# Optimization experiments

Measured on AMD Instinct MI355X. Metric: run time of the kernel, lower is better.

## Reference

```python
import math
import jax, jax.numpy as jnp
import numpy as np

B, L, HID = 2, 2048, 2048
H = 16
D = HID // H  # 128
EPS = 1e-6
ROPE_BASE = 10000.0
BETA_MIN, BETA_MAX = 0.8, 0.9995


def _rope_cache(seq_len, dim):
    half = dim // 2
    inv_freq = 1.0 / (ROPE_BASE ** (jnp.arange(half, dtype=jnp.float32) / float(half)))
    t = jnp.arange(seq_len, dtype=jnp.float32)
    freqs = t[:, None] * inv_freq[None, :]  # [L, half]
    return jnp.cos(freqs), jnp.sin(freqs)


def _apply_rope(x, cos, sin):
    # x: [B, H, L, D]; cos/sin: [L, D//2]
    half = x.shape[-1] // 2
    xe, xo = x[..., :half], x[..., half:]
    c = cos[None, None]
    s = sin[None, None]
    return jnp.concatenate([xe * c - xo * s, xe * s + xo * c], axis=-1)


def setup_inputs() -> dict:
    key = jax.random.key(0)
    ks = jax.random.split(key, 6)
    sc = 1.0 / math.sqrt(HID)  # ~ xavier scale
    return {
        "x": jax.random.normal(ks[0], (B, L, HID), jnp.float32),
        "Wq": jax.random.normal(ks[1], (HID, HID), jnp.float32) * sc,
        "Wk": jax.random.normal(ks[2], (HID, HID), jnp.float32) * sc,
        "Wv": jax.random.normal(ks[3], (HID, HID), jnp.float32) * sc,
        "Wg": jax.random.normal(ks[4], (HID, H), jnp.float32) * sc,
        "bg": jnp.full((H,), math.log(0.98 / (1.0 - 0.98)), jnp.float32),
        "Wo": jax.random.normal(ks[5], (HID, HID), jnp.float32) * sc,
        "bo": jnp.zeros((HID,), jnp.float32),
    }


def _deltanet(x, Wq, Wk, Wv, Wg, bg, Wo, bo):
    Bb, Ll, _ = x.shape
    split = lambda t: t.reshape(Bb, Ll, H, D).transpose(0, 2, 1, 3)  # [B,H,L,D]
    q = split(x @ Wq)
    k = split(x @ Wk)
    v = split(x @ Wv)

    cos, sin = _rope_cache(Ll, D)
    q = _apply_rope(q, cos, sin)
    k = _apply_rope(k, cos, sin)

    beta = jax.nn.sigmoid(x @ Wg + bg)                # [B,L,H]
    beta = jnp.clip(beta, BETA_MIN, BETA_MAX).transpose(0, 2, 1)  # [B,H,L]

    phi_q = jax.nn.elu(q) + 1.0
    phi_k = jax.nn.elu(k) + 1.0

    # time-major for scan
    pq = phi_q.transpose(2, 0, 1, 3)  # [L,B,H,D]
    pk = phi_k.transpose(2, 0, 1, 3)
    vt = v.transpose(2, 0, 1, 3)
    bt = beta.transpose(2, 0, 1)      # [L,B,H]

    S0 = jnp.zeros((Bb, H, D, D), jnp.float32)
    z0 = jnp.zeros((Bb, H, D), jnp.float32)

    def step(carry, inp):
        S, z = carry
        pq_t, pk_t, v_t, b_t = inp
        S = S * b_t[..., None, None] + pk_t[..., :, None] * v_t[..., None, :]
        z = z * b_t[..., None] + pk_t
        numer = jnp.einsum('bhd,bhde->bhe', pq_t, S)
        denom = jnp.sum(pq_t * z, axis=-1, keepdims=True) + EPS
        return (S, z), numer / denom

    (_, _), y = jax.lax.scan(step, (S0, z0), (pq, pk, vt, bt))  # y: [L,B,H,D]
    y = y.transpose(1, 0, 2, 3).reshape(Bb, Ll, HID)  # [B,L,H*D]
    return y @ Wo + bo


def reference(x, Wq, Wk, Wv, Wg, bg, Wo, bo):
    return _deltanet(x, Wq, Wk, Wv, Wg, bg, Wo, bo)
```

## Files before the change

### kernel.cpp

```cpp
#include <hip/hip_runtime.h>


typedef __attribute__((ext_vector_type(8))) short short8;
typedef __attribute__((ext_vector_type(4))) float f32x4;

__device__ __forceinline__ unsigned short f2bf(float f) {
  unsigned u = __float_as_uint(f);
  u += 0x7fffu + ((u >> 16) & 1u);
  return (unsigned short)(u >> 16);
}
__device__ __forceinline__ float bf2f(unsigned short s) {
  return __uint_as_float(((unsigned)s) << 16);
}
__device__ __forceinline__ float phi_elu1(float x) {
  return x > 0.f ? x + 1.f : expf(x);
}
__device__ __forceinline__ void gl_lds16(const void* g, void* l) {
  __builtin_amdgcn_global_load_lds(
      (const __attribute__((address_space(1))) void*)g,
      (__attribute__((address_space(3))) void*)l, 16, 0, 0);
}

__global__ __launch_bounds__(256)
void k_cast(const float* __restrict__ x, unsigned short* __restrict__ xb) {
  int i = (blockIdx.x * 256 + threadIdx.x) * 4;
  float4 f = *(const float4*)(x + i);
  uint2 p;
  p.x = (unsigned)f2bf(f.x) | ((unsigned)f2bf(f.y) << 16);
  p.y = (unsigned)f2bf(f.z) | ((unsigned)f2bf(f.w) << 16);
  *(uint2*)(xb + i) = p;
}

__global__ __launch_bounds__(256)
void k_transw(const float* __restrict__ Wq, const float* __restrict__ Wk,
              const float* __restrict__ Wv, const float* __restrict__ Wo,
              const float* __restrict__ Wg,
              unsigned short* __restrict__ Wt, unsigned short* __restrict__ Wot,
              unsigned short* __restrict__ Wgt16) {
  const int z = blockIdx.z;
  if (z == 4) {
    if (blockIdx.y != 0) return;
    int idx = blockIdx.x * 256 + threadIdx.x;
    int h = idx >> 9, k4 = (idx & 511) * 4;
    uint2 p;
    p.x = (unsigned)f2bf(Wg[(k4 + 0) * 16 + h]) | ((unsigned)f2bf(Wg[(k4 + 1) * 16 + h]) << 16);
    p.y = (unsigned)f2bf(Wg[(k4 + 2) * 16 + h]) | ((unsigned)f2bf(Wg[(k4 + 3) * 16 + h]) << 16);
    *(uint2*)(Wgt16 + (size_t)h * 2048 + k4) = p;
    return;
  }
  const float* W = (z == 0) ? Wq : (z == 1) ? Wk : (z == 2) ? Wv : Wo;
  unsigned short* out = (z < 3) ? (Wt + (size_t)z * 2048 * 2048) : Wot;
  __shared__ float tile[64][65];
  const int n0 = blockIdx.x * 64;
  const int k0 = blockIdx.y * 64;
  const int tx = threadIdx.x & 63;
  const int ty = threadIdx.x >> 6;
#pragma unroll
  for (int rl = 0; rl < 16; ++rl) {
    int kk = rl * 4 + ty;
    tile[kk][tx] = W[(size_t)(k0 + kk) * 2048 + n0 + tx];
  }
  __syncthreads();
#pragma unroll
  for (int rl = 0; rl < 16; ++rl) {
    int nn = rl * 4 + ty;
    out[(size_t)(n0 + nn) * 2048 + k0 + tx] = f2bf(tile[tx][nn]);
  }
}

__global__ __launch_bounds__(256)
void k_betaW(const unsigned short* __restrict__ xb, const unsigned short* __restrict__ Wgt16,
             const float* __restrict__ bg, float* __restrict__ beta) {
  const int w = threadIdx.x >> 6;
  const int lane = threadIdx.x & 63;
  const int m = blockIdx.x * 4 + w;
  const int h = lane & 15, kq = lane >> 4;
  const unsigned short* xr = xb + (size_t)m * 2048 + kq * 512;
  const unsigned short* wr = Wgt16 + (size_t)h * 2048 + kq * 512;
  float acc = 0.f;
#pragma unroll 8
  for (int i = 0; i < 64; ++i) {
    short8 xv = *(const short8*)(xr + i * 8);
    short8 wv = *(const short8*)(wr + i * 8);
#pragma unroll
    for (int j = 0; j < 8; ++j)
      acc = fmaf(bf2f((unsigned short)xv[j]), bf2f((unsigned short)wv[j]), acc);
  }
  acc += __shfl_xor(acc, 16, 64);
  acc += __shfl_xor(acc, 32, 64);
  if (lane < 16) {
    float v = acc + bg[h];
    float bv = 1.f / (1.f + expf(-v));
    beta[(size_t)m * 16 + h] = fminf(fmaxf(bv, 0.8f), 0.9995f);
  }
}

template <bool OUT_BF16, bool ADD_BIAS>
__global__ __launch_bounds__(256)
void k_gemm(const unsigned short* __restrict__ A, const unsigned short* __restrict__ Bt,
            void* __restrict__ Cptr, const float* __restrict__ bias,
            int M, int N, int K, int ldA, int ldC) {
  __shared__ __align__(16) unsigned short As[128][64];
  __shared__ __align__(16) unsigned short Bs[128][64];
  const int tid = threadIdx.x;
  const int n0 = blockIdx.x * 128;
  const int m0 = blockIdx.y * 128;
  const int lane = tid & 63;
  const int w = tid >> 6;
  const int wm = w >> 1, wn = w & 1;
  const int q = lane >> 4, r = lane & 15;

  const int srow0 = w * 8 + (lane >> 3);
  const int scol = ((lane & 7) ^ ((lane >> 3) & 7)) * 8;

  f32x4 acc[4][4];
#pragma unroll
  for (int i = 0; i < 4; ++i)
#pragma unroll
    for (int j = 0; j < 4; ++j) acc[i][j] = (f32x4){0.f, 0.f, 0.f, 0.f};

  const unsigned short* A0 = A + (size_t)(m0 + srow0) * ldA + scol;
  const unsigned short* B0 = Bt + (size_t)(n0 + srow0) * K + scol;
  unsigned short* lA = &As[srow0][(lane & 7) * 8];
  unsigned short* lB = &Bs[srow0][(lane & 7) * 8];

  const int rsw = r & 7;

  for (int kt = 0; kt < K; kt += 64) {
    __syncthreads();
#pragma unroll
    for (int i = 0; i < 4; ++i) {
      gl_lds16(A0 + (size_t)i * 32 * ldA + kt, lA + i * 2048);
      gl_lds16(B0 + (size_t)i * 32 * K + kt, lB + i * 2048);
    }
    __syncthreads();
#pragma unroll
    for (int kk = 0; kk < 2; ++kk) {
      const int ps = ((kk * 4 + q) ^ rsw) * 8;
      short8 af[4], bfr[4];
#pragma unroll
      for (int i = 0; i < 4; ++i)
        af[i] = *(const short8*)&As[wm * 64 + i * 16 + r][ps];
#pragma unroll
      for (int j = 0; j < 4; ++j)
        bfr[j] = *(const short8*)&Bs[wn * 64 + j * 16 + r][ps];
#pragma unroll
      for (int i = 0; i < 4; ++i)
#pragma unroll
        for (int j = 0; j < 4; ++j)
          acc[i][j] = __builtin_amdgcn_mfma_f32_16x16x32_bf16(af[i], bfr[j], acc[i][j], 0, 0, 0);
    }
  }
#pragma unroll
  for (int i = 0; i < 4; ++i) {
#pragma unroll
    for (int j = 0; j < 4; ++j) {
#pragma unroll
      for (int rr = 0; rr < 4; ++rr) {
        int mi = m0 + wm * 64 + i * 16 + q * 4 + rr;
        int ni = n0 + wn * 64 + j * 16 + r;
        float val = acc[i][j][rr];
        if (ADD_BIAS) val += bias[ni];
        if (OUT_BF16)
          ((unsigned short*)Cptr)[(size_t)mi * ldC + ni] = f2bf(val);
        else
          ((float*)Cptr)[(size_t)mi * ldC + ni] = val;
      }
    }
  }
}

__global__ __launch_bounds__(256)
void k_prep(const unsigned short* __restrict__ qkv, const float* __restrict__ beta,
            unsigned short* __restrict__ Qt, unsigned short* __restrict__ Ktg,
            unsigned short* __restrict__ Ag, float* __restrict__ gch) {
  const int ch = blockIdx.x;
  const int bh = blockIdx.y;
  const int b = bh >> 4, h = bh & 15;
  const int tid = threadIdx.x;
  const int t0 = ch * 64;

  __shared__ float Gs[64];
  __shared__ unsigned short Qs[64][136];
  __shared__ unsigned short Ks[64][136];

  if (tid < 64) {
    float bb = beta[((size_t)(b * 2048 + t0 + tid)) * 16 + h];
#pragma unroll
    for (int off = 1; off < 64; off <<= 1) {
      float o = __shfl_up(bb, off, 64);
      if (tid >= off) bb *= o;
    }
    Gs[tid] = bb;
    if (tid == 63) gch[bh * 32 + ch] = bb;
  }
  __syncthreads();

  const int dgl = tid & 7;
  float invf[8];
#pragma unroll
  for (int j = 0; j < 8; ++j)
    invf[j] = expf((float)(dgl * 8 + j) * -0.14391156831212787f);

  int s = tid >> 3;
#pragma unroll
  for (int rep = 0; rep < 2; ++rep, s += 32) {
    size_t row = ((size_t)(b * 2048 + t0 + s)) * 6144 + (size_t)h * 128;
    short8 qlo = *(const short8*)(qkv + row + dgl * 8);
    short8 qhi = *(const short8*)(qkv + row + 64 + dgl * 8);
    short8 klo = *(const short8*)(qkv + row + 2048 + dgl * 8);
    short8 khi = *(const short8*)(qkv + row + 2048 + 64 + dgl * 8);
    float g = Gs[s];
    float ig = 1.f / g;
    float tg = (float)(t0 + s);
    short8 oql, oqh, okl, okh;
#pragma unroll
    for (int j = 0; j < 8; ++j) {
      float sn, cs;
      __sincosf(tg * invf[j], &sn, &cs);
      float qe = bf2f((unsigned short)qlo[j]), qo = bf2f((unsigned short)qhi[j]);
      float a0 = qe * cs - qo * sn, a1 = qe * sn + qo * cs;
      oql[j] = (short)f2bf(phi_elu1(a0) * g);
      oqh[j] = (short)f2bf(phi_elu1(a1) * g);
      float ke = bf2f((unsigned short)klo[j]), ko = bf2f((unsigned short)khi[j]);
      a0 = ke * cs - ko * sn;
      a1 = ke * sn + ko * cs;
      okl[j] = (short)f2bf(phi_elu1(a0) * ig);
      okh[j] = (short)f2bf(phi_elu1(a1) * ig);
    }
    size_t qbase = (((size_t)bh * 32 + ch) * 64 + s) * 128;
    *(short8*)(Qt + qbase + dgl * 8) = oql;
    *(short8*)(Qt + qbase + 64 + dgl * 8) = oqh;
    *(short8*)&Qs[s][dgl * 8] = oql;
    *(short8*)&Qs[s][64 + dgl * 8] = oqh;
    *(short8*)&Ks[s][dgl * 8] = okl;
    *(short8*)&Ks[s][64 + dgl * 8] = okh;
  }
  __syncthreads();

  {
    const int d = tid >> 1, sh = tid & 1;
    unsigned pk[16];
#pragma unroll
    for (int i = 0; i < 16; ++i)
      pk[i] = (unsigned)Ks[sh * 32 + 2 * i][d] | ((unsigned)Ks[sh * 32 + 2 * i + 1][d] << 16);
    unsigned short* kr = Ktg + ((size_t)bh * 32 + ch) * 8192 + (size_t)d * 64 + sh * 32;
#pragma unroll
    for (int i = 0; i < 4; ++i)
      *(uint4*)(kr + i * 8) = *(uint4*)&pk[i * 4];
  }

  {
    const int lane = tid & 63;
    const int w = tid >> 6;
    const int q = lane >> 4, r = lane & 15;
    f32x4 acc[4];
#pragma unroll
    for (int nt = 0; nt < 4; ++nt) acc[nt] = (f32x4){0.f, 0.f, 0.f, 0.f};
#pragma unroll
    for (int kk = 0; kk < 4; ++kk) {
      short8 af = *(const short8*)&Qs[w * 16 + r][kk * 32 + q * 8];
#pragma unroll
      for (int nt = 0; nt < 4; ++nt) {
        short8 bf = *(const short8*)&Ks[nt * 16 + r][kk * 32 + q * 8];
        acc[nt] = __builtin_amdgcn_mfma_f32_16x16x32_bf16(af, bf, acc[nt], 0, 0, 0);
      }
    }
    unsigned short* Agp = Ag + ((size_t)bh * 32 + ch) * 4096;
#pragma unroll
    for (int nt = 0; nt < 4; ++nt) {
#pragma unroll
      for (int rr = 0; rr < 4; ++rr) {
        int t_l = w * 16 + q * 4 + rr;
        int s_l = nt * 16 + r;
        float val = (s_l <= t_l) ? acc[nt][rr] : 0.f;
        Agp[t_l * 64 + s_l] = f2bf(val);
      }
    }
  }
}

__global__ __launch_bounds__(256)
void k_scan(const unsigned short* __restrict__ Qt, const unsigned short* __restrict__ Ktg,
            const unsigned short* __restrict__ Ag, const unsigned short* __restrict__ qkv,
            const float* __restrict__ gch, unsigned short* __restrict__ numerb) {
  const int eb = blockIdx.x;
  const int bh = blockIdx.y;
  const int b = bh >> 4, h = bh & 15;
  const int tid = threadIdx.x;
  const int lane = tid & 63;
  const int w = tid >> 6;
  const int q = lane >> 4, r = lane & 15;
  const int e0 = eb * 16;

  __shared__ unsigned short Qs[64][136];
  __shared__ unsigned short Kts[128][72];
  __shared__ unsigned short As[64][72];
  __shared__ unsigned short Vt[16][72];
  __shared__ unsigned short SbT[16][136];
  __shared__ __align__(16) float zbuf[2][128];

  f32x4 S_acc[2];
  S_acc[0] = (f32x4){0.f, 0.f, 0.f, 0.f};
  S_acc[1] = (f32x4){0.f, 0.f, 0.f, 0.f};
  if (tid < 128) zbuf[0][tid] = 0.f;

  for (int ch = 0; ch < 32; ++ch) {
    const int cur = ch & 1, nxt = cur ^ 1;
    __syncthreads();
    {
      const unsigned short* Qg = Qt + ((size_t)bh * 32 + ch) * 8192;
#pragma unroll
      for (int i = 0; i < 4; ++i) {
        int c = tid + i * 256;
        int ss = c >> 4, dg = c & 15;
        *(int4*)&Qs[ss][dg * 8] = *(const int4*)(Qg + ss * 128 + dg * 8);
      }
      const unsigned short* Kg = Ktg + ((size_t)bh * 32 + ch) * 8192;
#pragma unroll
      for (int i = 0; i < 4; ++i) {
        int c = tid + i * 256;
        int d = c >> 3, sg = c & 7;
        *(int4*)&Kts[d][sg * 8] = *(const int4*)(Kg + d * 64 + sg * 8);
      }
      const unsigned short* Agp = Ag + ((size_t)bh * 32 + ch) * 4096;
#pragma unroll
      for (int i = 0; i < 2; ++i) {
        int c = tid + i * 256;
        int t_l = c >> 3, sg = c & 7;
        *(int4*)&As[t_l][sg * 8] = *(const int4*)(Agp + t_l * 64 + sg * 8);
      }
      {
        int ss = tid >> 2, e4 = tid & 3;
        const unsigned short* vp =
            qkv + ((size_t)(b * 2048 + ch * 64 + ss)) * 6144 + 4096 + h * 128 + e0 + e4 * 4;
        uint2 vv = *(const uint2*)vp;
        const unsigned short* pv = (const unsigned short*)&vv;
#pragma unroll
        for (int j = 0; j < 4; ++j) Vt[e4 * 4 + j][ss] = pv[j];
      }
#pragma unroll
      for (int i = 0; i < 2; ++i)
#pragma unroll
        for (int rr = 0; rr < 4; ++rr)
          SbT[r][(2 * w + i) * 16 + q * 4 + rr] = f2bf(S_acc[i][rr]);
    }
    __syncthreads();

    const float gc = gch[bh * 32 + ch];

    f32x4 nacc = (f32x4){0.f, 0.f, 0.f, 0.f};
    float dsum = 0.f;
#pragma unroll
    for (int kk = 0; kk < 4; ++kk) {
      short8 af = *(const short8*)&Qs[w * 16 + r][kk * 32 + q * 8];
      short8 bf = *(const short8*)&SbT[r][kk * 32 + q * 8];
      nacc = __builtin_amdgcn_mfma_f32_16x16x32_bf16(af, bf, nacc, 0, 0, 0);
      const float* zp = &zbuf[cur][kk * 32 + q * 8];
      float4 z0a = *(const float4*)zp;
      float4 z0b = *(const float4*)(zp + 4);
      dsum = fmaf(bf2f((unsigned short)af[0]), z0a.x, dsum);
      dsum = fmaf(bf2f((unsigned short)af[1]), z0a.y, dsum);
      dsum = fmaf(bf2f((unsigned short)af[2]), z0a.z, dsum);
      dsum = fmaf(bf2f((unsigned short)af[3]), z0a.w, dsum);
      dsum = fmaf(bf2f((unsigned short)af[4]), z0b.x, dsum);
      dsum = fmaf(bf2f((unsigned short)af[5]), z0b.y, dsum);
      dsum = fmaf(bf2f((unsigned short)af[6]), z0b.z, dsum);
      dsum = fmaf(bf2f((unsigned short)af[7]), z0b.w, dsum);
    }
    short8 vf[2];
#pragma unroll
    for (int kk = 0; kk < 2; ++kk) {
      vf[kk] = *(const short8*)&Vt[r][kk * 32 + q * 8];
      short8 af = *(const short8*)&As[w * 16 + r][kk * 32 + q * 8];
      nacc = __builtin_amdgcn_mfma_f32_16x16x32_bf16(af, vf[kk], nacc, 0, 0, 0);
#pragma unroll
      for (int j = 0; j < 8; ++j) dsum += bf2f((unsigned short)af[j]);
    }
    dsum += __shfl_xor(dsum, 16, 64);
    dsum += __shfl_xor(dsum, 32, 64);
    float inv = 1.f / (dsum + 1e-6f);
#pragma unroll
    for (int rr = 0; rr < 4; ++rr) {
      float inv_r = __shfl(inv, q * 4 + rr, 64);
      int t_l = w * 16 + q * 4 + rr;
      size_t m = (size_t)b * 2048 + ch * 64 + t_l;
      numerb[m * 2048 + h * 128 + e0 + r] = f2bf(nacc[rr] * inv_r);
    }

    {
      int d = tid >> 1, half = tid & 1;
      const unsigned short* kp = &Kts[d][half * 32];
      float zs = 0.f;
#pragma unroll
      for (int i = 0; i < 4; ++i) {
        short8 kv = *(const short8*)(kp + i * 8);
#pragma unroll
        for (int j = 0; j < 8; ++j) zs += bf2f((unsigned short)kv[j]);
      }
      zs += __shfl_xor(zs, 1, 64);
      if (half == 0) zbuf[nxt][d] = gc * (zbuf[cur][d] + zs);
    }

#pragma unroll
    for (int i = 0; i < 2; ++i) {
#pragma unroll
      for (int kk = 0; kk < 2; ++kk) {
        short8 af = *(const short8*)&Kts[(2 * w + i) * 16 + r][kk * 32 + q * 8];
        S_acc[i] = __builtin_amdgcn_mfma_f32_16x16x32_bf16(af, vf[kk], S_acc[i], 0, 0, 0);
      }
#pragma unroll
      for (int rr = 0; rr < 4; ++rr) S_acc[i][rr] *= gc;
    }
  }
}

extern "C" void kernel_launch(void* const* d_in, const int* in_sizes, int n_in,
                              void* d_out, int out_size, void* d_ws, size_t ws_size,
                              hipStream_t stream) {
  const float* x  = (const float*)d_in[0];
  const float* Wq = (const float*)d_in[1];
  const float* Wk = (const float*)d_in[2];
  const float* Wv = (const float*)d_in[3];
  const float* Wg = (const float*)d_in[4];
  const float* bg = (const float*)d_in[5];
  const float* Wo = (const float*)d_in[6];
  const float* bo = (const float*)d_in[7];

  char* ws = (char*)d_ws;
  unsigned short* xb    = (unsigned short*)(ws);
  unsigned short* Qt    = (unsigned short*)(ws);
  unsigned short* Wt    = (unsigned short*)(ws + 16777216);
  unsigned short* Ktg   = (unsigned short*)(ws + 16777216);
  unsigned short* Ag    = (unsigned short*)(ws + 33554432);
  unsigned short* Wot   = (unsigned short*)(ws + 41943040);
  unsigned short* qkvb  = (unsigned short*)(ws + 50331648);
  float*          beta  = (float*)(ws + 100663296);
  unsigned short* Wgt16 = (unsigned short*)(ws + 101187584);
  unsigned short* numerb= (unsigned short*)(ws + 101187584);
  float*          gch   = (float*)d_out;

  k_cast<<<8192, 256, 0, stream>>>(x, xb);
  k_transw<<<dim3(32, 32, 5), 256, 0, stream>>>(Wq, Wk, Wv, Wo, Wg, Wt, Wot, Wgt16);
  k_gemm<true, false><<<dim3(48, 32), 256, 0, stream>>>(
      xb, Wt, qkvb, nullptr, 4096, 6144, 2048, 2048, 6144);
  k_betaW<<<1024, 256, 0, stream>>>(xb, Wgt16, bg, beta);
  k_prep<<<dim3(32, 32), 256, 0, stream>>>(qkvb, beta, Qt, Ktg, Ag, gch);
  k_scan<<<dim3(8, 32), 256, 0, stream>>>(Qt, Ktg, Ag, qkvb, gch, numerb);
  k_gemm<false, true><<<dim3(16, 32), 256, 0, stream>>>(
      numerb, Wot, d_out, bo, 4096, 2048, 2048, 2048, 2048);
}
```

Baseline: 427.7 us.

## Use 256x256-tile 512-thread pipelined GEMM for the QKV projection

Adds a new bf16 MFMA GEMM kernel with 256x256 output tiles, 8 waves, double-buffered LDS loaded via global_load_lds, XOR-swizzled layout, and staged prefetch interleaved with compute in four sub-phases. The large QKV projection is switched to it, which raises data reuse per tile and overlaps loads with MFMA work. In exchange the grid is smaller (384 blocks), so SM fill and tail effects matter, register pressure is higher with 128 accumulator floats per thread, and there are more barriers per K-step.

```diff
diff --git a/kernel.cpp b/kernel.cpp
--- a/kernel.cpp
+++ b/kernel.cpp
@@ -19,6 +19,11 @@
   __builtin_amdgcn_global_load_lds(
       (const __attribute__((address_space(1))) void*)g,
       (__attribute__((address_space(3))) void*)l, 16, 0, 0);
+}
+__device__ __forceinline__ void bar_raw() {
+  asm volatile("" ::: "memory");
+  __builtin_amdgcn_s_barrier();
+  asm volatile("" ::: "memory");
 }
 
 __global__ __launch_bounds__(256)
@@ -170,6 +175,117 @@
   }
 }
 
+template <bool OUT_BF16, bool ADD_BIAS>
+__global__ __launch_bounds__(512, 2)
+void k_gemm256(const unsigned short* __restrict__ A, const unsigned short* __restrict__ Bt,
+               void* __restrict__ Cptr, const float* __restrict__ bias,
+               int M, int N, int K, int ldA, int ldC) {
+  __shared__ __align__(16) unsigned short Ls[2][4][128][64];
+  const int tid = threadIdx.x;
+  const int lane = tid & 63;
+  const int w = tid >> 6;
+  const int wm = w >> 2;
+  const int wn = w & 3;
+  const int ql = lane >> 4;
+  const int r = lane & 15;
+  const int n0 = blockIdx.x * 256;
+  const int m0 = blockIdx.y * 256;
+
+  const int srow = tid >> 3;
+  const int sphys = tid & 7;
+  const int slog = sphys ^ (srow & 7);
+  const unsigned short* Abase = A + (size_t)(m0 + srow) * ldA + slog * 8;
+  const unsigned short* Bbase = Bt + (size_t)(n0 + srow) * K + slog * 8;
+
+#define STAGE256(Xv)                                                          \
+  do {                                                                        \
+    const int Xh = (Xv);                                                      \
+    const int tx = Xh >> 2, jx = Xh & 3;                                      \
+    const size_t ldx = (jx < 2) ? (size_t)K : (size_t)ldA;                    \
+    const unsigned short* gsrc =                                              \
+        ((jx < 2) ? Bbase : Abase) + (size_t)((jx & 1) * 128) * ldx +         \
+        (size_t)tx * 64;                                                      \
+    unsigned short* ldst = &Ls[tx & 1][jx ^ 2][srow][sphys * 8];              \
+    gl_lds16(gsrc, ldst);                                                     \
+    gl_lds16(gsrc + 64 * ldx, ldst + 64 * 64);                                \
+  } while (0)
+
+  f32x4 acc[8][4];
+#pragma unroll
+  for (int i = 0; i < 8; ++i)
+#pragma unroll
+    for (int j = 0; j < 4; ++j) acc[i][j] = (f32x4){0.f, 0.f, 0.f, 0.f};
+
+  const int NT = K >> 6;
+
+  for (int X = 0; X < 6; ++X) STAGE256(X);
+  asm volatile("s_waitcnt vmcnt(4)" ::: "memory");
+  bar_raw();
+
+  short8 bfr[4][2];
+
+  for (int t = 0; t < NT; ++t) {
+    const int slt = t & 1;
+    const unsigned short (*LA)[64] = Ls[slt][wm];
+    const unsigned short (*LB)[64] = Ls[slt][2 + (wn >> 1)];
+    const int brow0 = (wn & 1) * 64;
+#pragma unroll
+    for (int p = 0; p < 4; ++p) {
+      if (p == 0) {
+#pragma unroll
+        for (int nj = 0; nj < 4; ++nj)
+#pragma unroll
+          for (int kk = 0; kk < 2; ++kk)
+            bfr[nj][kk] = *(const short8*)
+                &LB[brow0 + nj * 16 + r][((kk * 4 + ql) ^ (r & 7)) * 8];
+      }
+      short8 af[2][2];
+#pragma unroll
+      for (int im = 0; im < 2; ++im)
+#pragma unroll
+        for (int kk = 0; kk < 2; ++kk)
+          af[im][kk] = *(const short8*)
+              &LA[(2 * p + im) * 16 + r][((kk * 4 + ql) ^ (r & 7)) * 8];
+      {
+        const int X = 4 * t + p + 6;
+        if (X < 4 * NT) STAGE256(X);
+      }
+      bar_raw();
+      __builtin_amdgcn_s_setprio(1);
+#pragma unroll
+      for (int kk = 0; kk < 2; ++kk)
+#pragma unroll
+        for (int im = 0; im < 2; ++im)
+#pragma unroll
+          for (int nj = 0; nj < 4; ++nj)
+            acc[2 * p + im][nj] = __builtin_amdgcn_mfma_f32_16x16x32_bf16(
+                af[im][kk], bfr[nj][kk], acc[2 * p + im][nj], 0, 0, 0);
+      __builtin_amdgcn_s_setprio(0);
+      if (p == 3) asm volatile("s_waitcnt vmcnt(4)" ::: "memory");
+      bar_raw();
+    }
+  }
+#undef STAGE256
+
+#pragma unroll
+  for (int mi = 0; mi < 8; ++mi) {
+#pragma unroll
+    for (int nj = 0; nj < 4; ++nj) {
+#pragma unroll
+      for (int rr = 0; rr < 4; ++rr) {
+        int mrow = m0 + wm * 128 + mi * 16 + ql * 4 + rr;
+        int ncol = n0 + wn * 64 + nj * 16 + r;
+        float val = acc[mi][nj][rr];
+        if (ADD_BIAS) val += bias[ncol];
+        if (OUT_BF16)
+          ((unsigned short*)Cptr)[(size_t)mrow * ldC + ncol] = f2bf(val);
+        else
+          ((float*)Cptr)[(size_t)mrow * ldC + ncol] = val;
+      }
+    }
+  }
+}
+
 __global__ __launch_bounds__(256)
 void k_prep(const unsigned short* __restrict__ qkv, const float* __restrict__ beta,
             unsigned short* __restrict__ Qt, unsigned short* __restrict__ Ktg,
@@ -442,7 +558,7 @@
 
   k_cast<<<8192, 256, 0, stream>>>(x, xb);
   k_transw<<<dim3(32, 32, 5), 256, 0, stream>>>(Wq, Wk, Wv, Wo, Wg, Wt, Wot, Wgt16);
-  k_gemm<true, false><<<dim3(48, 32), 256, 0, stream>>>(
+  k_gemm256<true, false><<<dim3(24, 16), 512, 0, stream>>>(
       xb, Wt, qkvb, nullptr, 4096, 6144, 2048, 2048, 6144);
   k_betaW<<<1024, 256, 0, stream>>>(xb, Wgt16, bg, beta);
   k_prep<<<dim3(32, 32), 256, 0, stream>>>(qkvb, beta, Qt, Ktg, Ag, gch);
```

Result: no change. 427.5 us (-0.0%).

## Rewrite GEMM with 256x128 tiles, triple-buffered LDS pipeline and block swizzle

Applied to the files above, without the earlier changes.

Replaces the 128x128 single-buffered GEMM with a 512-thread kernel computing 256x128 tiles. It uses a three-stage LDS ring filled with global_load_lds prefetches two k-tiles ahead, raw barriers with explicit vmcnt waits, and setprio around MFMA bursts. Block indices are remapped so neighbouring workgroups share tiles for L2 reuse. The goal is to hide global load latency behind MFMA work and cut synchronisation stalls, at the cost of more LDS (about 144KB per block) and fragile hand-tuned waitcnt logic.

```diff
diff --git a/kernel.cpp b/kernel.cpp
--- a/kernel.cpp
+++ b/kernel.cpp
@@ -19,6 +19,11 @@
   __builtin_amdgcn_global_load_lds(
       (const __attribute__((address_space(1))) void*)g,
       (__attribute__((address_space(3))) void*)l, 16, 0, 0);
+}
+__device__ __forceinline__ void bar_raw() {
+  asm volatile("" ::: "memory");
+  __builtin_amdgcn_s_barrier();
+  asm volatile("" ::: "memory");
 }
 
 __global__ __launch_bounds__(256)
@@ -96,22 +101,41 @@
 }
 
 template <bool OUT_BF16, bool ADD_BIAS>
-__global__ __launch_bounds__(256)
-void k_gemm(const unsigned short* __restrict__ A, const unsigned short* __restrict__ Bt,
-            void* __restrict__ Cptr, const float* __restrict__ bias,
-            int M, int N, int K, int ldA, int ldC) {
-  __shared__ __align__(16) unsigned short As[128][64];
-  __shared__ __align__(16) unsigned short Bs[128][64];
+__global__ __launch_bounds__(512, 2)
+void k_gemm2(const unsigned short* __restrict__ A, const unsigned short* __restrict__ Bt,
+             void* __restrict__ Cptr, const float* __restrict__ bias,
+             int M, int N, int K, int ldA, int ldC) {
+  __shared__ __align__(16) unsigned short Ls[3][3][128][64];
   const int tid = threadIdx.x;
-  const int n0 = blockIdx.x * 128;
-  const int m0 = blockIdx.y * 128;
   const int lane = tid & 63;
   const int w = tid >> 6;
-  const int wm = w >> 1, wn = w & 1;
-  const int q = lane >> 4, r = lane & 15;
-
-  const int srow0 = w * 8 + (lane >> 3);
-  const int scol = ((lane & 7) ^ ((lane >> 3) & 7)) * 8;
+  const int wm = w >> 1;
+  const int wn = w & 1;
+  const int ql = lane >> 4;
+  const int r = lane & 15;
+
+  const int nwg = gridDim.x * gridDim.y;
+  const int orig = blockIdx.y * gridDim.x + blockIdx.x;
+  const int li = (orig & 7) * (nwg >> 3) + (orig >> 3);
+  const int m0 = (li & 15) * 256;
+  const int n0 = (li >> 4) * 128;
+
+  const int srow = tid >> 3;
+  const int sphys = tid & 7;
+  const int slog = sphys ^ (srow & 7);
+  const unsigned short* Ab = A + (size_t)(m0 + srow) * ldA + slog * 8;
+  const unsigned short* Bb = Bt + (size_t)(n0 + srow) * K + slog * 8;
+
+#define STG(st, h, tt)                                                        \
+  do {                                                                        \
+    const size_t ldx = ((h) == 2) ? (size_t)K : (size_t)ldA;                  \
+    const unsigned short* gs =                                                \
+        (((h) == 2) ? Bb : (Ab + (size_t)((h) * 128) * ldA)) +                \
+        (size_t)(tt) * 64;                                                    \
+    unsigned short* ld = &Ls[(st)][(h)][srow][sphys * 8];                     \
+    gl_lds16(gs, ld);                                                         \
+    gl_lds16(gs + 64 * ldx, ld + 64 * 64);                                    \
+  } while (0)
 
   f32x4 acc[4][4];
 #pragma unroll
@@ -119,52 +143,88 @@
 #pragma unroll
     for (int j = 0; j < 4; ++j) acc[i][j] = (f32x4){0.f, 0.f, 0.f, 0.f};
 
-  const unsigned short* A0 = A + (size_t)(m0 + srow0) * ldA + scol;
-  const unsigned short* B0 = Bt + (size_t)(n0 + srow0) * K + scol;
-  unsigned short* lA = &As[srow0][(lane & 7) * 8];
-  unsigned short* lB = &Bs[srow0][(lane & 7) * 8];
-
-  const int rsw = r & 7;
-
-  for (int kt = 0; kt < K; kt += 64) {
-    __syncthreads();
-#pragma unroll
-    for (int i = 0; i < 4; ++i) {
-      gl_lds16(A0 + (size_t)i * 32 * ldA + kt, lA + i * 2048);
-      gl_lds16(B0 + (size_t)i * 32 * K + kt, lB + i * 2048);
-    }
-    __syncthreads();
-#pragma unroll
-    for (int kk = 0; kk < 2; ++kk) {
-      const int ps = ((kk * 4 + q) ^ rsw) * 8;
-      short8 af[4], bfr[4];
-#pragma unroll
-      for (int i = 0; i < 4; ++i)
-        af[i] = *(const short8*)&As[wm * 64 + i * 16 + r][ps];
-#pragma unroll
-      for (int j = 0; j < 4; ++j)
-        bfr[j] = *(const short8*)&Bs[wn * 64 + j * 16 + r][ps];
-#pragma unroll
-      for (int i = 0; i < 4; ++i)
-#pragma unroll
-        for (int j = 0; j < 4; ++j)
-          acc[i][j] = __builtin_amdgcn_mfma_f32_16x16x32_bf16(af[i], bfr[j], acc[i][j], 0, 0, 0);
-    }
-  }
-#pragma unroll
-  for (int i = 0; i < 4; ++i) {
-#pragma unroll
-    for (int j = 0; j < 4; ++j) {
+  const int NT = K >> 6;
+
+#pragma unroll
+  for (int h = 0; h < 3; ++h) STG(0, h, 0);
+#pragma unroll
+  for (int h = 0; h < 3; ++h) STG(1, h, 1);
+  asm volatile("s_waitcnt vmcnt(6)" ::: "memory");
+  bar_raw();
+
+  short8 bfr[4][2];
+
+  for (int t = 0; t < NT; ++t) {
+    const int st = t % 3;
+    const unsigned short (*LA)[64] = Ls[st][wm >> 1];
+    const unsigned short (*LB)[64] = Ls[st][2];
+    const int arow0 = (wm & 1) * 64;
+    const int brow0 = wn * 64;
+    const bool pf = (t + 2 < NT);
+    const int s2 = (t + 2) % 3;
+#pragma unroll
+    for (int p = 0; p < 2; ++p) {
+      if (p == 0) {
+#pragma unroll
+        for (int nj = 0; nj < 4; ++nj)
+#pragma unroll
+          for (int kk = 0; kk < 2; ++kk)
+            bfr[nj][kk] = *(const short8*)
+                &LB[brow0 + nj * 16 + r][((kk * 4 + ql) ^ (r & 7)) * 8];
+      }
+      short8 af[2][2];
+#pragma unroll
+      for (int im = 0; im < 2; ++im)
+#pragma unroll
+        for (int kk = 0; kk < 2; ++kk)
+          af[im][kk] = *(const short8*)
+              &LA[arow0 + (p * 2 + im) * 16 + r][((kk * 4 + ql) ^ (r & 7)) * 8];
+      if (pf) {
+        if (p == 0) {
+          STG(s2, 0, t + 2);
+          STG(s2, 1, t + 2);
+        } else {
+          STG(s2, 2, t + 2);
+        }
+      }
+      bar_raw();
+      asm volatile("s_waitcnt lgkmcnt(0)" ::: "memory");
+      __builtin_amdgcn_sched_barrier(0);
+      __builtin_amdgcn_s_setprio(1);
+#pragma unroll
+      for (int kk = 0; kk < 2; ++kk)
+#pragma unroll
+        for (int im = 0; im < 2; ++im)
+#pragma unroll
+          for (int nj = 0; nj < 4; ++nj)
+            acc[p * 2 + im][nj] = __builtin_amdgcn_mfma_f32_16x16x32_bf16(
+                af[im][kk], bfr[nj][kk], acc[p * 2 + im][nj], 0, 0, 0);
+      __builtin_amdgcn_s_setprio(0);
+      if (p == 1) {
+        if (pf)
+          asm volatile("s_waitcnt vmcnt(6)" ::: "memory");
+        else if (t + 1 < NT)
+          asm volatile("s_waitcnt vmcnt(0)" ::: "memory");
+      }
+      bar_raw();
+    }
+  }
+#undef STG
+
+#pragma unroll
+  for (int mi = 0; mi < 4; ++mi) {
+#pragma unroll
+    for (int nj = 0; nj < 4; ++nj) {
 #pragma unroll
       for (int rr = 0; rr < 4; ++rr) {
-        int mi = m0 + wm * 64 + i * 16 + q * 4 + rr;
-        int ni = n0 + wn * 64 + j * 16 + r;
-        float val = acc[i][j][rr];
-        if (ADD_BIAS) val += bias[ni];
+        int mrow = m0 + wm * 64 + mi * 16 + ql * 4 + rr;
+        int ncol = n0 + wn * 64 + nj * 16 + r;
+        float val = acc[mi][nj][rr];
+        if (ADD_BIAS) val += bias[ncol];
         if (OUT_BF16)
-          ((unsigned short*)Cptr)[(size_t)mi * ldC + ni] = f2bf(val);
+          ((unsigned short*)Cptr)[(size_t)mrow * ldC + ncol] = f2bf(val);
         else
-          ((float*)Cptr)[(size_t)mi * ldC + ni] = val;
+          ((float*)Cptr)[(size_t)mrow * ldC + ncol] = val;
       }
     }
   }
@@ -442,11 +502,11 @@
 
   k_cast<<<8192, 256, 0, stream>>>(x, xb);
   k_transw<<<dim3(32, 32, 5), 256, 0, stream>>>(Wq, Wk, Wv, Wo, Wg, Wt, Wot, Wgt16);
-  k_gemm<true, false><<<dim3(48, 32), 256, 0, stream>>>(
+  k_gemm2<true, false><<<dim3(16, 48), 512, 0, stream>>>(
       xb, Wt, qkvb, nullptr, 4096, 6144, 2048, 2048, 6144);
   k_betaW<<<1024, 256, 0, stream>>>(xb, Wgt16, bg, beta);
   k_prep<<<dim3(32, 32), 256, 0, stream>>>(qkvb, beta, Qt, Ktg, Ag, gch);
   k_scan<<<dim3(8, 32), 256, 0, stream>>>(Qt, Ktg, Ag, qkvb, gch, numerb);
-  k_gemm<false, true><<<dim3(16, 32), 256, 0, stream>>>(
+  k_gemm2<false, true><<<dim3(16, 16), 512, 0, stream>>>(
       numerb, Wot, d_out, bo, 4096, 2048, 2048, 2048, 2048);
 }
```

Result: no change. 426.6 us (-0.2%).
